# Kernel tuning notes

Hardware: AMD Instinct MI355X
Metric: run time of the kernel (lower is better)

## Reference

```python
import jax, jax.numpy as jnp
import numpy as np

T = 10.0
DIVISOR = 3.0
K = 2
LAMBDA_ALPHA = 1.0
LAMBDA_BETA = 0.5


def setup_inputs() -> dict:
    key = jax.random.key(0)
    ks = jax.random.split(key, 5)
    N, C, H, W = 32, 64, 112, 112
    R = 8
    hidden = C // R
    x = jax.random.normal(ks[0], (N, C, H, W), dtype=jnp.float32)
    conv_w = jax.random.normal(ks[1], (C,), dtype=jnp.float32) * 0.1
    conv_b = jnp.zeros((1,), dtype=jnp.float32)
    w1 = jax.random.normal(ks[2], (C, hidden), dtype=jnp.float32) * 0.1
    b1 = jnp.zeros((hidden,), dtype=jnp.float32)
    w2 = jax.random.normal(ks[3], (hidden, 2 * K * C), dtype=jnp.float32) * 0.1
    b2 = jnp.zeros((2 * K * C,), dtype=jnp.float32)
    return {"x": x, "conv_w": conv_w, "conv_b": conv_b,
            "w1": w1, "b1": b1, "w2": w2, "b2": b2}


def reference(x, conv_w, conv_b, w1, b1, w2, b2):
    N, C, H, W = x.shape
    gamma = (H * W) / DIVISOR

    # Spatial attention: 1x1 conv C->1, per-sample softmax over HW, scale+clamp.
    s = jnp.einsum('nchw,c->nhw', x, conv_w) + conv_b[0]          # [N,H,W]
    p = jax.nn.softmax((s / T).reshape(N, -1), axis=-1)            # [N,HW]
    spatial = jnp.minimum(gamma * p, 1.0).reshape(N, 1, H, W)      # [N,1,H,W]

    # Residual head (DyReLU-C coefficient branch): GAP -> FC -> ReLU -> FC -> 2*sigmoid-1.
    pooled = x.mean(axis=(2, 3))                                   # [N,C]
    h = jax.nn.relu(pooled @ w1 + b1)                              # [N,C//R]
    theta = 2.0 * jax.nn.sigmoid(h @ w2 + b2) - 1.0                # [N,2*K*C]
    theta = theta.reshape(N, K, C, 2)
    alpha = theta[..., 0]                                          # [N,K,C]
    beta = theta[..., 1]                                           # [N,K,C]

    init_alpha = jnp.array([1.0, 0.0], dtype=x.dtype)              # K=2
    init_beta = jnp.array([1.0, 0.0], dtype=x.dtype)
    a = init_alpha[None, :, None] + LAMBDA_ALPHA * alpha           # [N,K,C]
    b = init_beta[None, :, None] + LAMBDA_BETA * beta              # [N,K,C]

    # result_k = spatial * (x * a_k + b_k); max over k branches.
    out_k = spatial[:, None] * (x[:, None] * a[..., None, None] + b[..., None, None])
    return jnp.max(out_k, axis=1)                                  # [N,C,H,W]
```

## Files before the change

kernel.cpp:

```cpp
#include <hip/hip_runtime.h>
#include <math.h>

#define NN 32
#define CC 64
#define HWD 12544
#define HW4 3136
#define HID 8
#define OUTD 256
#define T_INV 0.1f
#define GAMMA_F (12544.0f / 3.0f)
#define PIECES 13

typedef float v4f __attribute__((ext_vector_type(4)));

__device__ __forceinline__ float wave_sum(float v) {
    #pragma unroll
    for (int off = 32; off; off >>= 1) v += __shfl_down(v, off, 64);
    return v;
}

__global__ __launch_bounds__(256) void k1_stats(const float* __restrict__ x,
        const float* __restrict__ cw, const float* __restrict__ cb,
        float* __restrict__ pp, float* __restrict__ se) {
    __shared__ float w[CC];
    __shared__ float pool_lds[4][CC];
    __shared__ float se_lds[4];
    int tid = threadIdx.x, lane = tid & 63, wv = tid >> 6;
    int n = blockIdx.x / PIECES, piece = blockIdx.x % PIECES;
    if (tid < CC) w[tid] = cw[tid];
    __syncthreads();

    int i = piece * 256 + tid;
    bool act = i < HW4;
    const float4* x4 = (const float4*)x + (long)n * CC * HW4;

    float p64[64];
    #pragma unroll
    for (int c = 0; c < CC; c++) p64[c] = 0.f;
    float4 cacc = make_float4(0.f, 0.f, 0.f, 0.f);

    if (act) {
        #pragma unroll
        for (int c = 0; c < CC; c++) {
            float4 v = x4[(long)c * HW4 + i];
            float ww = w[c];
            cacc.x += v.x * ww; cacc.y += v.y * ww;
            cacc.z += v.z * ww; cacc.w += v.w * ww;
            p64[c] = (v.x + v.y) + (v.z + v.w);
        }
    }
    float bb = cb[0];
    float se_acc = 0.f;
    if (act) {
        se_acc = __expf((cacc.x + bb) * T_INV) + __expf((cacc.y + bb) * T_INV)
               + __expf((cacc.z + bb) * T_INV) + __expf((cacc.w + bb) * T_INV);
    }

    #pragma unroll
    for (int c = 0; c < CC; c++) p64[c] = wave_sum(p64[c]);
    se_acc = wave_sum(se_acc);
    if (lane == 0) {
        #pragma unroll
        for (int c = 0; c < CC; c++) pool_lds[wv][c] = p64[c];
        se_lds[wv] = se_acc;
    }
    __syncthreads();
    if (tid < CC)
        pp[(n * PIECES + piece) * CC + tid] = pool_lds[0][tid] + pool_lds[1][tid]
                                            + pool_lds[2][tid] + pool_lds[3][tid];
    if (tid == 0)
        se[n * PIECES + piece] = se_lds[0] + se_lds[1] + se_lds[2] + se_lds[3];
}

__global__ __launch_bounds__(256) void k2_mlp(const float* __restrict__ pp,
        const float* __restrict__ se, const float* __restrict__ w1,
        const float* __restrict__ b1, const float* __restrict__ w2,
        const float* __restrict__ b2, float* __restrict__ a_ws,
        float* __restrict__ b_ws, float* __restrict__ scale) {
    int n = blockIdx.x, t = threadIdx.x;
    __shared__ float p[CC];
    __shared__ float h[HID];
    if (t < CC) {
        float acc = 0.f;
        #pragma unroll
        for (int piece = 0; piece < PIECES; piece++)
            acc += pp[(n * PIECES + piece) * CC + t];
        p[t] = acc * (1.0f / HWD);
    }
    if (t == 0) {
        float ss = 0.f;
        #pragma unroll
        for (int piece = 0; piece < PIECES; piece++) ss += se[n * PIECES + piece];
        scale[n] = GAMMA_F / ss;
    }
    __syncthreads();
    if (t < HID) {
        float acc = b1[t];
        #pragma unroll 8
        for (int c = 0; c < CC; c++) acc += p[c] * w1[c * HID + t];
        h[t] = fmaxf(acc, 0.f);
    }
    __syncthreads();
    float o = b2[t];
    #pragma unroll
    for (int j = 0; j < HID; j++) o += h[j] * w2[j * OUTD + t];
    float theta = 2.f / (1.f + __expf(-o)) - 1.f;
    int k = t >> 7, c = (t >> 1) & 63, d = t & 1;
    float init = (k == 0) ? 1.f : 0.f;
    int idx = n * 128 + k * 64 + c;
    if (d == 0) a_ws[idx] = init + theta;
    else        b_ws[idx] = init + 0.5f * theta;
}

__global__ __launch_bounds__(256) void k3_final(const float* __restrict__ x,
        const float* __restrict__ cw, const float* __restrict__ cb,
        const float* __restrict__ a_ws, const float* __restrict__ b_ws,
        const float* __restrict__ scale, float* __restrict__ out) {
    __shared__ float w[CC];
    __shared__ float A0[CC], B0[CC], A1[CC], B1[CC];
    int tid = threadIdx.x;
    int n = blockIdx.x / PIECES, piece = blockIdx.x % PIECES;
    if (tid < CC) {
        w[tid]  = cw[tid];
        A0[tid] = a_ws[n * 128 + tid];
        B0[tid] = b_ws[n * 128 + tid];
        A1[tid] = a_ws[n * 128 + 64 + tid];
        B1[tid] = b_ws[n * 128 + 64 + tid];
    }
    __syncthreads();
    int i = piece * 256 + tid;
    if (i >= HW4) return;

    const float4* x4 = (const float4*)x + (long)n * CC * HW4;
    float4 cacc = make_float4(0.f, 0.f, 0.f, 0.f);
    #pragma unroll
    for (int c = 0; c < CC; c++) {
        float4 v = x4[(long)c * HW4 + i];
        float ww = w[c];
        cacc.x += v.x * ww; cacc.y += v.y * ww;
        cacc.z += v.z * ww; cacc.w += v.w * ww;
    }
    float bb = cb[0], sc = scale[n];
    float4 sp;
    sp.x = fminf(sc * __expf((cacc.x + bb) * T_INV), 1.f);
    sp.y = fminf(sc * __expf((cacc.y + bb) * T_INV), 1.f);
    sp.z = fminf(sc * __expf((cacc.z + bb) * T_INV), 1.f);
    sp.w = fminf(sc * __expf((cacc.w + bb) * T_INV), 1.f);

    v4f* o4 = (v4f*)out + (long)n * CC * HW4;
    #pragma unroll 8
    for (int c = 0; c < CC; c++) {
        float4 v = x4[(long)c * HW4 + i];
        float a0 = A0[c], b0 = B0[c], a1 = A1[c], b1v = B1[c];
        v4f r;
        r.x = sp.x * fmaxf(v.x * a0 + b0, v.x * a1 + b1v);
        r.y = sp.y * fmaxf(v.y * a0 + b0, v.y * a1 + b1v);
        r.z = sp.z * fmaxf(v.z * a0 + b0, v.z * a1 + b1v);
        r.w = sp.w * fmaxf(v.w * a0 + b0, v.w * a1 + b1v);
        __builtin_nontemporal_store(r, &o4[(long)c * HW4 + i]);
    }
}

extern "C" void kernel_launch(void* const* d_in, const int* in_sizes, int n_in,
                              void* d_out, int out_size, void* d_ws, size_t ws_size,
                              hipStream_t stream) {
    const float* x      = (const float*)d_in[0];
    const float* conv_w = (const float*)d_in[1];
    const float* conv_b = (const float*)d_in[2];
    const float* w1     = (const float*)d_in[3];
    const float* b1     = (const float*)d_in[4];
    const float* w2     = (const float*)d_in[5];
    const float* b2     = (const float*)d_in[6];
    float* out = (float*)d_out;

    float* ws   = (float*)d_ws;
    float* pp   = ws;
    float* se   = pp + NN * PIECES * CC;
    float* a_ws = se + NN * PIECES;
    float* b_ws = a_ws + NN * 2 * CC;
    float* scl  = b_ws + NN * 2 * CC;

    k1_stats<<<NN * PIECES, 256, 0, stream>>>(x, conv_w, conv_b, pp, se);
    k2_mlp  <<<NN,          256, 0, stream>>>(pp, se, w1, b1, w2, b2, a_ws, b_ws, scl);
    k3_final<<<NN * PIECES, 256, 0, stream>>>(x, conv_w, conv_b, a_ws, b_ws, scl, out);
}
```

Baseline: 232.2 us.

## Cache spatial exp map in workspace and flatten final pass to elementwise

The stats kernel now runs one 64-lane wave per 256-pixel chunk, writes the per-pixel exp of the conv score to a workspace buffer, and reduces the 64 channel pool sums with a butterfly transpose instead of 64 separate wave reductions plus LDS. The final kernel no longer recomputes the 64-channel conv dot product. It becomes a flat elementwise pass over all output float4s that reads x, the cached exp map and per-channel coefficients. This removes the extra pass over x in the final kernel and raises parallelism, at the cost of writing and rereading a small exp buffer and doing per-thread integer divisions and scattered coefficient loads.

Result: faster. 214.3 us (-7.7%).

```diff
diff --git a/kernel.cpp b/kernel.cpp
--- a/kernel.cpp
+++ b/kernel.cpp
@@ -5,11 +5,13 @@
 #define CC 64
 #define HWD 12544
 #define HW4 3136
+#define CHUNKS_PER_N 49
+#define NCHUNK (NN * CHUNKS_PER_N)
 #define HID 8
 #define OUTD 256
 #define T_INV 0.1f
 #define GAMMA_F (12544.0f / 3.0f)
-#define PIECES 13
+#define TOT4 (NN * CC * HW4)
 
 typedef float v4f __attribute__((ext_vector_type(4)));
 
@@ -19,57 +21,59 @@
     return v;
 }
 
-__global__ __launch_bounds__(256) void k1_stats(const float* __restrict__ x,
+__global__ __launch_bounds__(64) void k1_stats(const float* __restrict__ x,
         const float* __restrict__ cw, const float* __restrict__ cb,
-        float* __restrict__ pp, float* __restrict__ se) {
-    __shared__ float w[CC];
-    __shared__ float pool_lds[4][CC];
-    __shared__ float se_lds[4];
-    int tid = threadIdx.x, lane = tid & 63, wv = tid >> 6;
-    int n = blockIdx.x / PIECES, piece = blockIdx.x % PIECES;
-    if (tid < CC) w[tid] = cw[tid];
-    __syncthreads();
+        float* __restrict__ pp, float* __restrict__ se,
+        float* __restrict__ ews) {
+    int lane = threadIdx.x;
+    int g = blockIdx.x;
+    int n = g / CHUNKS_PER_N;
+    int j = g - n * CHUNKS_PER_N;
 
-    int i = piece * 256 + tid;
-    bool act = i < HW4;
-    const float4* x4 = (const float4*)x + (long)n * CC * HW4;
+    const float4* x4 = (const float4*)x + (size_t)n * CC * HW4 + j * 64 + lane;
 
     float p64[64];
+    float4 cacc = make_float4(0.f, 0.f, 0.f, 0.f);
     #pragma unroll
-    for (int c = 0; c < CC; c++) p64[c] = 0.f;
-    float4 cacc = make_float4(0.f, 0.f, 0.f, 0.f);
-
-    if (act) {
-        #pragma unroll
-        for (int c = 0; c < CC; c++) {
-            float4 v = x4[(long)c * HW4 + i];
-            float ww = w[c];
-            cacc.x += v.x * ww; cacc.y += v.y * ww;
-            cacc.z += v.z * ww; cacc.w += v.w * ww;
-            p64[c] = (v.x + v.y) + (v.z + v.w);
-        }
-    }
-    float bb = cb[0];
-    float se_acc = 0.f;
-    if (act) {
-        se_acc = __expf((cacc.x + bb) * T_INV) + __expf((cacc.y + bb) * T_INV)
-               + __expf((cacc.z + bb) * T_INV) + __expf((cacc.w + bb) * T_INV);
+    for (int c = 0; c < CC; ++c) {
+        float4 v = x4[(size_t)c * HW4];
+        float ww = cw[c];
+        cacc.x += v.x * ww; cacc.y += v.y * ww;
+        cacc.z += v.z * ww; cacc.w += v.w * ww;
+        p64[c] = (v.x + v.y) + (v.z + v.w);
     }
 
-    #pragma unroll
-    for (int c = 0; c < CC; c++) p64[c] = wave_sum(p64[c]);
-    se_acc = wave_sum(se_acc);
-    if (lane == 0) {
-        #pragma unroll
-        for (int c = 0; c < CC; c++) pool_lds[wv][c] = p64[c];
-        se_lds[wv] = se_acc;
+    float bb = cb[0];
+    float4 e;
+    e.x = __expf((cacc.x + bb) * T_INV);
+    e.y = __expf((cacc.y + bb) * T_INV);
+    e.z = __expf((cacc.z + bb) * T_INV);
+    e.w = __expf((cacc.w + bb) * T_INV);
+    ((float4*)ews)[(size_t)n * HW4 + j * 64 + lane] = e;
+
+    float se_acc = wave_sum((e.x + e.y) + (e.z + e.w));
+    if (lane == 0) se[g] = se_acc;
+
+    #define BFLY_ROUND(S, LEN)                                         \
+    {                                                                  \
+        bool up = (lane >> (S)) & 1;                                   \
+        _Pragma("unroll")                                              \
+        for (int q = 0; q < (LEN); ++q) {                              \
+            float send = up ? p64[q] : p64[q + (LEN)];                 \
+            float recv = __shfl_xor(send, 1 << (S), 64);               \
+            p64[q] = (up ? p64[q + (LEN)] : p64[q]) + recv;            \
+        }                                                              \
     }
-    __syncthreads();
-    if (tid < CC)
-        pp[(n * PIECES + piece) * CC + tid] = pool_lds[0][tid] + pool_lds[1][tid]
-                                            + pool_lds[2][tid] + pool_lds[3][tid];
-    if (tid == 0)
-        se[n * PIECES + piece] = se_lds[0] + se_lds[1] + se_lds[2] + se_lds[3];
+    BFLY_ROUND(0, 32)
+    BFLY_ROUND(1, 16)
+    BFLY_ROUND(2, 8)
+    BFLY_ROUND(3, 4)
+    BFLY_ROUND(4, 2)
+    BFLY_ROUND(5, 1)
+    #undef BFLY_ROUND
+
+    int ch = (int)(__brev((unsigned)lane) >> 26);
+    pp[g * CC + ch] = p64[0];
 }
 
 __global__ __launch_bounds__(256) void k2_mlp(const float* __restrict__ pp,
@@ -83,27 +87,27 @@
     if (t < CC) {
         float acc = 0.f;
         #pragma unroll
-        for (int piece = 0; piece < PIECES; piece++)
-            acc += pp[(n * PIECES + piece) * CC + t];
+        for (int j = 0; j < CHUNKS_PER_N; ++j)
+            acc += pp[(n * CHUNKS_PER_N + j) * CC + t];
         p[t] = acc * (1.0f / HWD);
     }
     if (t == 0) {
         float ss = 0.f;
         #pragma unroll
-        for (int piece = 0; piece < PIECES; piece++) ss += se[n * PIECES + piece];
+        for (int j = 0; j < CHUNKS_PER_N; ++j) ss += se[n * CHUNKS_PER_N + j];
         scale[n] = GAMMA_F / ss;
     }
     __syncthreads();
     if (t < HID) {
         float acc = b1[t];
         #pragma unroll 8
-        for (int c = 0; c < CC; c++) acc += p[c] * w1[c * HID + t];
+        for (int c = 0; c < CC; ++c) acc += p[c] * w1[c * HID + t];
         h[t] = fmaxf(acc, 0.f);
     }
     __syncthreads();
     float o = b2[t];
     #pragma unroll
-    for (int j = 0; j < HID; j++) o += h[j] * w2[j * OUTD + t];
+    for (int j = 0; j < HID; ++j) o += h[j] * w2[j * OUTD + t];
     float theta = 2.f / (1.f + __expf(-o)) - 1.f;
     int k = t >> 7, c = (t >> 1) & 63, d = t & 1;
     float init = (k == 0) ? 1.f : 0.f;
@@ -113,52 +117,34 @@
 }
 
 __global__ __launch_bounds__(256) void k3_final(const float* __restrict__ x,
-        const float* __restrict__ cw, const float* __restrict__ cb,
-        const float* __restrict__ a_ws, const float* __restrict__ b_ws,
-        const float* __restrict__ scale, float* __restrict__ out) {
-    __shared__ float w[CC];
-    __shared__ float A0[CC], B0[CC], A1[CC], B1[CC];
-    int tid = threadIdx.x;
-    int n = blockIdx.x / PIECES, piece = blockIdx.x % PIECES;
-    if (tid < CC) {
-        w[tid]  = cw[tid];
-        A0[tid] = a_ws[n * 128 + tid];
-        B0[tid] = b_ws[n * 128 + tid];
-        A1[tid] = a_ws[n * 128 + 64 + tid];
-        B1[tid] = b_ws[n * 128 + 64 + tid];
-    }
-    __syncthreads();
-    int i = piece * 256 + tid;
-    if (i >= HW4) return;
+        const float* __restrict__ ews, const float* __restrict__ a_ws,
+        const float* __restrict__ b_ws, const float* __restrict__ scale,
+        float* __restrict__ out) {
+    unsigned f = blockIdx.x * 256u + threadIdx.x;
+    unsigned n = f / (CC * HW4);
+    unsigned r = f - n * (CC * HW4);
+    unsigned c = r / HW4;
+    unsigned g = r - c * HW4;
 
-    const float4* x4 = (const float4*)x + (long)n * CC * HW4;
-    float4 cacc = make_float4(0.f, 0.f, 0.f, 0.f);
-    #pragma unroll
-    for (int c = 0; c < CC; c++) {
-        float4 v = x4[(long)c * HW4 + i];
-        float ww = w[c];
-        cacc.x += v.x * ww; cacc.y += v.y * ww;
-        cacc.z += v.z * ww; cacc.w += v.w * ww;
-    }
-    float bb = cb[0], sc = scale[n];
-    float4 sp;
-    sp.x = fminf(sc * __expf((cacc.x + bb) * T_INV), 1.f);
-    sp.y = fminf(sc * __expf((cacc.y + bb) * T_INV), 1.f);
-    sp.z = fminf(sc * __expf((cacc.z + bb) * T_INV), 1.f);
-    sp.w = fminf(sc * __expf((cacc.w + bb) * T_INV), 1.f);
+    float4 v = ((const float4*)x)[f];
+    float4 e = ((const float4*)ews)[n * HW4 + g];
+    float sc = scale[n];
+    float a0 = a_ws[n * 128 + c];
+    float a1 = a_ws[n * 128 + 64 + c];
+    float b0 = b_ws[n * 128 + c];
+    float b1v = b_ws[n * 128 + 64 + c];
 
-    v4f* o4 = (v4f*)out + (long)n * CC * HW4;
-    #pragma unroll 8
-    for (int c = 0; c < CC; c++) {
-        float4 v = x4[(long)c * HW4 + i];
-        float a0 = A0[c], b0 = B0[c], a1 = A1[c], b1v = B1[c];
-        v4f r;
-        r.x = sp.x * fmaxf(v.x * a0 + b0, v.x * a1 + b1v);
-        r.y = sp.y * fmaxf(v.y * a0 + b0, v.y * a1 + b1v);
-        r.z = sp.z * fmaxf(v.z * a0 + b0, v.z * a1 + b1v);
-        r.w = sp.w * fmaxf(v.w * a0 + b0, v.w * a1 + b1v);
-        __builtin_nontemporal_store(r, &o4[(long)c * HW4 + i]);
-    }
+    float spx = fminf(sc * e.x, 1.f);
+    float spy = fminf(sc * e.y, 1.f);
+    float spz = fminf(sc * e.z, 1.f);
+    float spw = fminf(sc * e.w, 1.f);
+
+    v4f r4;
+    r4.x = spx * fmaxf(v.x * a0 + b0, v.x * a1 + b1v);
+    r4.y = spy * fmaxf(v.y * a0 + b0, v.y * a1 + b1v);
+    r4.z = spz * fmaxf(v.z * a0 + b0, v.z * a1 + b1v);
+    r4.w = spw * fmaxf(v.w * a0 + b0, v.w * a1 + b1v);
+    __builtin_nontemporal_store(r4, &((v4f*)out)[f]);
 }
 
 extern "C" void kernel_launch(void* const* d_in, const int* in_sizes, int n_in,
@@ -175,12 +161,13 @@
 
     float* ws   = (float*)d_ws;
     float* pp   = ws;
-    float* se   = pp + NN * PIECES * CC;
-    float* a_ws = se + NN * PIECES;
+    float* se   = pp + NCHUNK * CC;
+    float* a_ws = se + NCHUNK;
     float* b_ws = a_ws + NN * 2 * CC;
     float* scl  = b_ws + NN * 2 * CC;
+    float* ews  = scl + NN;
 
-    k1_stats<<<NN * PIECES, 256, 0, stream>>>(x, conv_w, conv_b, pp, se);
-    k2_mlp  <<<NN,          256, 0, stream>>>(pp, se, w1, b1, w2, b2, a_ws, b_ws, scl);
-    k3_final<<<NN * PIECES, 256, 0, stream>>>(x, conv_w, conv_b, a_ws, b_ws, scl, out);
+    k1_stats<<<NCHUNK,      64, 0, stream>>>(x, conv_w, conv_b, pp, se, ews);
+    k2_mlp  <<<NN,         256, 0, stream>>>(pp, se, w1, b1, w2, b2, a_ws, b_ws, scl);
+    k3_final<<<TOT4 / 256, 256, 0, stream>>>(x, ews, a_ws, b_ws, scl, out);
 }
```
